# Kernel tuning notes

Measured on AMD Instinct MI355X. Metric: run time of the kernel, lower is better.

Reference implementation:

```python
import jax, jax.numpy as jnp
import numpy as np

NUM_HEADS = 8
CH_PER_HEAD = 32
NUM_GROUPS = 32
EPS = 1e-5
SCALE = CH_PER_HEAD ** (-0.25)


def setup_inputs() -> dict:
    key = jax.random.key(0)
    ks = jax.random.split(key, 6)
    B, C, H, W = 2, 256, 64, 64
    hid = NUM_HEADS * CH_PER_HEAD  # 256
    s = 1.0 / np.sqrt(C)
    return {
        "x": jax.random.normal(ks[0], (B, C, H, W), dtype=jnp.float32),
        "gamma": jnp.ones((C,), jnp.float32),
        "beta": jnp.zeros((C,), jnp.float32),
        "wq": jax.random.normal(ks[1], (hid, C), jnp.float32) * s,
        "bq": jnp.zeros((hid,), jnp.float32),
        "wk": jax.random.normal(ks[2], (hid, C), jnp.float32) * s,
        "bk": jnp.zeros((hid,), jnp.float32),
        "wv": jax.random.normal(ks[3], (hid, C), jnp.float32) * s,
        "bv": jnp.zeros((hid,), jnp.float32),
        "wout": jax.random.normal(ks[4], (C, hid), jnp.float32) * s,
        "bout": jnp.zeros((C,), jnp.float32),
    }


def _group_norm(x, gamma, beta):
    b, c, h, w = x.shape
    xg = x.reshape(b, NUM_GROUPS, c // NUM_GROUPS, h, w)
    mu = jnp.mean(xg, axis=(2, 3, 4), keepdims=True)
    var = jnp.var(xg, axis=(2, 3, 4), keepdims=True)
    xg = (xg - mu) * jax.lax.rsqrt(var + EPS)
    return xg.reshape(b, c, h, w) * gamma[None, :, None, None] + beta[None, :, None, None]


def reference(x, gamma, beta, wq, bq, wk, bk, wv, bv, wout, bout):
    b, c, h, w = x.shape
    n = h * w
    x_n = _group_norm(x, gamma, beta).reshape(b, c, n)  # b c n (self-attention: embedding = x_n)
    # 1x1 convs == pointwise linear over the channel dim
    q = jnp.einsum('oc,bcn->bon', wq, x_n) + bq[None, :, None]
    k = jnp.einsum('oc,bcn->bon', wk, x_n) + bk[None, :, None]
    v = jnp.einsum('oc,bcn->bon', wv, x_n) + bv[None, :, None]
    # split heads: b (h d) n -> b h d n
    d = CH_PER_HEAD
    q = q.reshape(b, NUM_HEADS, d, n)
    k = k.reshape(b, NUM_HEADS, d, n)
    v = v.reshape(b, NUM_HEADS, d, n)
    attn = jax.nn.softmax(jnp.einsum('bhdi,bhdj->bhij', q * SCALE, k * SCALE), axis=-1)
    out = jnp.einsum('bhij,bhdj->bhdi', attn, v).reshape(b, NUM_HEADS * d, n)
    out = jnp.einsum('oc,bcn->bon', wout, out) + bout[None, :, None]
    out = out.reshape(b, -1, h, w)
    return x + out  # shapes match -> residual
```

## Files before the change

### kernel.cpp

```cpp
#include <hip/hip_runtime.h>
#include <hip/hip_bf16.h>
#include <stdint.h>

typedef unsigned short u16;
typedef float f32x4 __attribute__((ext_vector_type(4)));
typedef float f32x16 __attribute__((ext_vector_type(16)));
typedef short bf16x8 __attribute__((ext_vector_type(8)));

#define NSP 4096
#define CDIM 256
#define HID 256
#define NH 8
#define DH 32
#define NG 32
#define CPG 8
#define BATCH 2
#define SPLIT 4
#define GN_EPS 1e-5f
#define QK2_SCALE 0.25503488f

#define MFMA32(A, B, C) __builtin_amdgcn_mfma_f32_32x32x16_bf16(A, B, C, 0, 0, 0)
#define MFMA16(A, B, C) __builtin_amdgcn_mfma_f32_16x16x32_bf16(A, B, C, 0, 0, 0)

__device__ __forceinline__ float bf2f(u16 u) {
    union { uint32_t i; float f; } v; v.i = ((uint32_t)u) << 16; return v.f;
}
__device__ __forceinline__ u16 f2bf(float f) {
    union { float f; uint32_t i; } v; v.f = f;
    uint32_t b = v.i;
    return (u16)((b + 0x7FFFu + ((b >> 16) & 1u)) >> 16);
}

__device__ __forceinline__ void gload16(const u16* g, u16* lds) {
    __builtin_amdgcn_global_load_lds(
        (const __attribute__((address_space(1))) uint32_t*)g,
        (__attribute__((address_space(3))) uint32_t*)lds, 16, 0, 0);
}

__device__ __forceinline__ void pl32swap(uint32_t& a, uint32_t& b) {
    asm("v_permlane32_swap_b32 %0, %1" : "+v"(a), "+v"(b));
}

__global__ void gn_stats(const float* __restrict__ x, float* __restrict__ stats,
                         const float* __restrict__ wq, const float* __restrict__ wk,
                         const float* __restrict__ wv, const float* __restrict__ wout,
                         u16* __restrict__ wcat) {
    int blk = blockIdx.x;
#pragma unroll
    for (int i = 0; i < 16; i++) {
        int idx = blk * 4096 + i * 256 + threadIdx.x;
        const float* src = (idx < 65536) ? wq : (idx < 131072) ? wk : (idx < 196608) ? wv : wout;
        wcat[idx] = f2bf(src[idx & 65535]);
    }
    const float4* base = (const float4*)(x + (size_t)blk * (CPG * NSP));
    float s = 0.f, ss = 0.f;
    for (int i = threadIdx.x; i < (CPG * NSP) / 4; i += 256) {
        float4 v = base[i];
        s  += v.x + v.y + v.z + v.w;
        ss += v.x * v.x + v.y * v.y + v.z * v.z + v.w * v.w;
    }
    for (int m = 1; m < 64; m <<= 1) { s += __shfl_xor(s, m, 64); ss += __shfl_xor(ss, m, 64); }
    __shared__ float ls[4], lss[4];
    int w = threadIdx.x >> 6;
    if ((threadIdx.x & 63) == 0) { ls[w] = s; lss[w] = ss; }
    __syncthreads();
    if (threadIdx.x == 0) {
        float S = ls[0] + ls[1] + ls[2] + ls[3];
        float SS = lss[0] + lss[1] + lss[2] + lss[3];
        float mean = S / (float)(CPG * NSP);
        float var = SS / (float)(CPG * NSP) - mean * mean;
        stats[2 * blk] = mean;
        stats[2 * blk + 1] = rsqrtf(var + GN_EPS);
    }
}

__global__ void gn_apply(const float* __restrict__ x, const float* __restrict__ stats,
                         const float* __restrict__ gamma, const float* __restrict__ beta,
                         u16* __restrict__ xn) {
    __shared__ u16 tile[64][72];
    int n0 = blockIdx.x * 64, c0 = blockIdx.y * 64, b = blockIdx.z;
    int t = threadIdx.x;
    int nl = t & 63, cq = t >> 6;
#pragma unroll
    for (int i = 0; i < 16; i++) {
        int cl = i * 4 + cq;
        int c = c0 + cl;
        int g = c >> 3;
        float mean = stats[2 * (b * NG + g)];
        float rstd = stats[2 * (b * NG + g) + 1];
        float v = x[((size_t)b * CDIM + c) * NSP + n0 + nl];
        v = (v - mean) * rstd * gamma[c] + beta[c];
        tile[cl][nl] = f2bf(v);
    }
    __syncthreads();
    int nr = t >> 2, cc = (t & 3) * 16;
    uint4 o0, o1;
    u16* p0 = (u16*)&o0; u16* p1 = (u16*)&o1;
#pragma unroll
    for (int j = 0; j < 8; j++) { p0[j] = tile[cc + j][nr]; p1[j] = tile[cc + 8 + j][nr]; }
    size_t orow = ((size_t)b * NSP + n0 + nr) * CDIM + c0 + cc;
    *(uint4*)(xn + orow) = o0;
    *(uint4*)(xn + orow + 8) = o1;
}

__global__ __launch_bounds__(256) void gemm_qkv(
    const u16* __restrict__ A, const u16* __restrict__ wcat,
    const float* __restrict__ bq, const float* __restrict__ bk, const float* __restrict__ bv,
    u16* __restrict__ qb, u16* __restrict__ kfb, u16* __restrict__ vfb) {
    __shared__ u16 As[128 * 64];
    __shared__ u16 Bs[128 * 64];
    int bz = blockIdx.z;
    const u16* Ab = A + (size_t)bz * NSP * CDIM;
    int n0 = blockIdx.x * 128, m0 = blockIdx.y * 128;
    int seg = n0 >> 8;
    int t = threadIdx.x, lane = t & 63, w = t >> 6;
    int wr = w >> 1, wc = w & 1;
    f32x4 acc[4][4] = {};

    int srow = w * 8 + (lane >> 3);
    int scol = (lane & 7) * 8;
    const u16* asrc = Ab + (size_t)(m0 + srow) * CDIM + scol;
    const u16* bsrc = wcat + (size_t)(n0 + srow) * CDIM + scol;
    u16* albase = As + w * 512;
    u16* blbase = Bs + w * 512;

    int frow = lane & 15, fcol = (lane >> 4) * 8;

    for (int k0 = 0; k0 < CDIM; k0 += 64) {
        __syncthreads();
#pragma unroll
        for (int ro = 0; ro < 4; ro++) {
            gload16(asrc + (size_t)ro * 32 * CDIM + k0, albase + ro * 2048);
            gload16(bsrc + (size_t)ro * 32 * CDIM + k0, blbase + ro * 2048);
        }
        asm volatile("s_waitcnt vmcnt(0)" ::: "memory");
        __syncthreads();
#pragma unroll
        for (int kk = 0; kk < 2; kk++) {
            bf16x8 af[4], bfv[4];
#pragma unroll
            for (int i = 0; i < 4; i++) {
                af[i]  = *(bf16x8*)&As[(wr * 64 + i * 16 + frow) * 64 + kk * 32 + fcol];
                bfv[i] = *(bf16x8*)&Bs[(wc * 64 + i * 16 + frow) * 64 + kk * 32 + fcol];
            }
#pragma unroll
            for (int i = 0; i < 4; i++)
#pragma unroll
                for (int j = 0; j < 4; j++)
                    acc[i][j] = MFMA16(af[i], bfv[j], acc[i][j]);
        }
    }

    const float* bias = (seg == 0) ? bq : (seg == 1) ? bk : bv;
    int r4 = (lane >> 4) * 4, cx = lane & 15;
#pragma unroll
    for (int i = 0; i < 4; i++) {
        int rbase = m0 + wr * 64 + i * 16 + r4;
#pragma unroll
        for (int j = 0; j < 4; j++) {
            int col = n0 + wc * 64 + j * 16 + cx;
            int cb = col & 255;
            float bb = bias[cb];
            if (seg == 0) {
#pragma unroll
                for (int r = 0; r < 4; r++)
                    qb[(size_t)bz * NSP * HID + (size_t)(rbase + r) * HID + cb] = f2bf(acc[i][j][r] + bb);
            } else if (seg == 1) {
                int h2 = cb >> 5;
                int f = 2 * ((rbase >> 5) & 1) + ((cb >> 4) & 1);
                size_t kt = ((size_t)(bz * NH + h2) * 64 + (rbase >> 6)) * 2048
                          + (size_t)f * 512 + ((rbase & 31) + (((cb >> 3) & 1) << 5)) * 8 + (cb & 7);
#pragma unroll
                for (int r = 0; r < 4; r++)
                    kfb[kt + r * 8] = f2bf((acc[i][j][r] + bb) * QK2_SCALE);
            } else {
                int h2 = cb >> 5, d = cb & 31;
                int jc = (rbase >> 3) & 7;
                size_t vt = ((size_t)(bz * NH + h2) * 64 + (rbase >> 6)) * 2048
                          + (size_t)(jc >> 1) * 512 + (d + ((jc & 1) << 5)) * 8 + (rbase & 7);
                uint2 pkd;
                pkd.x = ((uint32_t)f2bf(acc[i][j][1] + bb) << 16) | f2bf(acc[i][j][0] + bb);
                pkd.y = ((uint32_t)f2bf(acc[i][j][3] + bb) << 16) | f2bf(acc[i][j][2] + bb);
                *(uint2*)(vfb + vt) = pkd;
            }
        }
    }
}

__global__ __launch_bounds__(256) void gemm_out(
    const u16* __restrict__ A,
    const u16* __restrict__ B, long sB,
    const float* __restrict__ bias,
    const float* __restrict__ resid, long sR,
    float* __restrict__ outp, long sO,
    int N) {
    __shared__ u16 As[64][72];
    __shared__ u16 Bs[64][72];
    int bz = blockIdx.z;
    B += (size_t)bz * sB;
    int m0 = blockIdx.y * 64, n0 = blockIdx.x * 64;
    int t = threadIdx.x, lane = t & 63, w = t >> 6;
    int wm = (w >> 1) * 32, wn = (w & 1) * 32;
    f32x4 acc[2][2] = {};

    int sr = t >> 2;
    int sc1 = (t & 3) * 8, sc2 = sc1 + 32;

    uint4 av0 = *(const uint4*)(A + (size_t)(m0 + sr) * CDIM + sc1);
    uint4 av1 = *(const uint4*)(A + (size_t)(m0 + sr) * CDIM + sc2);
    uint4 bv0 = *(const uint4*)(B + (size_t)(n0 + sr) * CDIM + sc1);
    uint4 bv1 = *(const uint4*)(B + (size_t)(n0 + sr) * CDIM + sc2);

    for (int k0 = 0; k0 < CDIM; k0 += 64) {
        __syncthreads();
        *(uint4*)&As[sr][sc1] = av0;
        *(uint4*)&As[sr][sc2] = av1;
        *(uint4*)&Bs[sr][sc1] = bv0;
        *(uint4*)&Bs[sr][sc2] = bv1;
        __syncthreads();
        if (k0 + 64 < CDIM) {
            av0 = *(const uint4*)(A + (size_t)(m0 + sr) * CDIM + k0 + 64 + sc1);
            av1 = *(const uint4*)(A + (size_t)(m0 + sr) * CDIM + k0 + 64 + sc2);
            bv0 = *(const uint4*)(B + (size_t)(n0 + sr) * CDIM + k0 + 64 + sc1);
            bv1 = *(const uint4*)(B + (size_t)(n0 + sr) * CDIM + k0 + 64 + sc2);
        }
#pragma unroll
        for (int ks = 0; ks < 2; ks++) {
            bf16x8 af[2], bfr[2];
#pragma unroll
            for (int i = 0; i < 2; i++) {
                af[i]  = *(bf16x8*)&As[wm + i * 16 + (lane & 15)][ks * 32 + (lane >> 4) * 8];
                bfr[i] = *(bf16x8*)&Bs[wn + i * 16 + (lane & 15)][ks * 32 + (lane >> 4) * 8];
            }
#pragma unroll
            for (int i = 0; i < 2; i++)
#pragma unroll
                for (int j = 0; j < 2; j++)
                    acc[i][j] = MFMA16(af[i], bfr[j], acc[i][j]);
        }
    }

    int r4 = (lane >> 4) * 4, cx = lane & 15;
#pragma unroll
    for (int i = 0; i < 2; i++)
#pragma unroll
        for (int j = 0; j < 2; j++) {
            int rbase = m0 + wm + i * 16 + r4;
            int cbase = n0 + wn + j * 16 + cx;
#pragma unroll
            for (int r = 0; r < 4; r++) {
                int row = rbase + r, col = cbase;
                outp[(size_t)bz * sO + (size_t)row * N + col] =
                    acc[i][j][r] + bias[row] + resid[(size_t)bz * sR + (size_t)row * N + col];
            }
        }
}

__global__ __launch_bounds__(256, 4) void attn_kernel(
    const u16* __restrict__ q, const u16* __restrict__ kfb,
    const u16* __restrict__ vfb, u16* __restrict__ po, float* __restrict__ zz) {
    __shared__ float Ls[4][32];
    int h = blockIdx.y;
    int bz = blockIdx.z;
    int b = bz >> 2, sp = bz & 3;
    int kv0 = sp * (NSP / SPLIT);
    int t = threadIdx.x, lane = t & 63, w = t >> 6;
    int ql = lane & 31, hi = lane >> 5;
    int q0 = blockIdx.x * 128 + w * 32;

    const u16* qbp = q + (size_t)b * NSP * HID + (size_t)(q0 + ql) * HID + h * DH + hi * 8;
    bf16x8 qf0 = *(const bf16x8*)(qbp);
    bf16x8 qf1 = *(const bf16x8*)(qbp + 16);

    size_t tbase = ((size_t)(b * NH + h) * 64 + (kv0 >> 6)) * 2048 + (size_t)lane * 8;
    const u16* kp = kfb + tbase;
    const u16* vp = vfb + tbase;

#define LOADKF(kd, it) { \
    kd[0] = *(const bf16x8*)(kp + (size_t)(it) * 2048);        \
    kd[1] = *(const bf16x8*)(kp + (size_t)(it) * 2048 + 512);  \
    kd[2] = *(const bf16x8*)(kp + (size_t)(it) * 2048 + 1024); \
    kd[3] = *(const bf16x8*)(kp + (size_t)(it) * 2048 + 1536); }
#define LOADVF(vd, it) { \
    vd[0] = *(const bf16x8*)(vp + (size_t)(it) * 2048);        \
    vd[1] = *(const bf16x8*)(vp + (size_t)(it) * 2048 + 512);  \
    vd[2] = *(const bf16x8*)(vp + (size_t)(it) * 2048 + 1024); \
    vd[3] = *(const bf16x8*)(vp + (size_t)(it) * 2048 + 1536); }

    f32x16 kzero = {};
    f32x16 oacc = {};
    float l0 = 0.f, l1 = 0.f;

    auto process = [&](const bf16x8 (&kf)[4], const bf16x8 (&vf)[4]) {
#pragma unroll
        for (int tt = 0; tt < 2; tt++) {
            __builtin_amdgcn_s_setprio(1);
            f32x16 st = MFMA32(kf[2 * tt], qf0, kzero);
            st = MFMA32(kf[2 * tt + 1], qf1, st);
            __builtin_amdgcn_s_setprio(0);
            uint32_t pk[8];
#pragma unroll
            for (int j = 0; j < 8; j++) {
                float p0 = __builtin_amdgcn_exp2f(st[2 * j]);
                float p1 = __builtin_amdgcn_exp2f(st[2 * j + 1]);
                float ps = p0 + p1;
                if (j & 1) l1 += ps; else l0 += ps;
                uint32_t dd;
                asm("v_cvt_pk_bf16_f32 %0, %1, %2" : "=v"(dd) : "v"(p0), "v"(p1));
                pk[j] = dd;
            }
#pragma unroll
            for (int c = 0; c < 2; c++) {
                uint32_t a0 = pk[4 * c + 0], b0 = pk[4 * c + 2];
                uint32_t a1 = pk[4 * c + 1], b1 = pk[4 * c + 3];
                pl32swap(a0, b0);
                pl32swap(a1, b1);
                union { uint32_t u[4]; bf16x8 v8; } fr;
                fr.u[0] = a0; fr.u[1] = a1; fr.u[2] = b0; fr.u[3] = b1;
                __builtin_amdgcn_s_setprio(1);
                oacc = MFMA32(fr.v8, vf[2 * tt + c], oacc);
                __builtin_amdgcn_s_setprio(0);
            }
        }
    };

    const int NT = (NSP / SPLIT) / 64;
    bf16x8 ka[4], kc[4], va[4];
    LOADKF(ka, 0);
    for (int it = 0; it < NT; it += 2) {
        LOADVF(va, it);
        LOADKF(kc, it + 1);
        process(ka, va);
        LOADVF(va, it + 1);
        int n2 = (it + 2 < NT) ? it + 2 : 0;
        LOADKF(ka, n2);
        process(kc, va);
    }
#undef LOADKF
#undef LOADVF

    float l = l0 + l1;
    l += __shfl_xor(l, 32);
    Ls[w][ql] = 1.0f / l;
    if (hi == 0) zz[(((size_t)bz * NH + h) * NSP) + q0 + ql] = __log2f(l);
    u16* pob = po + ((((size_t)bz * NH + h) * NSP) + q0) * DH + ql;
#pragma unroll
    for (int r = 0; r < 16; r++) {
        int qq = (r & 3) + 8 * (r >> 2) + 4 * hi;
        pob[(size_t)qq * DH] = f2bf(oacc[r] * Ls[w][qq]);
    }
}

__global__ __launch_bounds__(256) void combine_kernel(
    const u16* __restrict__ po, const float* __restrict__ zz, u16* __restrict__ ao) {
    int idx = blockIdx.x * 256 + threadIdx.x;
    int c8 = idx & 31;
    int n  = (idx >> 5) & (NSP - 1);
    int b  = idx >> 17;
    int h  = c8 >> 2;
    int dp = (c8 & 3) * 8;

    float z[SPLIT];
    size_t base[SPLIT];
    float M = -3e38f;
#pragma unroll
    for (int s = 0; s < SPLIT; s++) {
        base[s] = ((((size_t)(b * SPLIT + s) * NH + h) * NSP) + n);
        z[s] = zz[base[s]];
        M = fmaxf(M, z[s]);
    }
    float wsum = 0.f, acc[8] = {};
#pragma unroll
    for (int s = 0; s < SPLIT; s++) {
        float ww = __builtin_amdgcn_exp2f(z[s] - M);
        wsum += ww;
        uint4 o = *(const uint4*)(po + base[s] * DH + dp);
        const u16* op = (const u16*)&o;
#pragma unroll
        for (int j = 0; j < 8; j++) acc[j] += bf2f(op[j]) * ww;
    }
    float inv = 1.0f / wsum;
    uint4 r;
    u16* rp = (u16*)&r;
#pragma unroll
    for (int j = 0; j < 8; j++) rp[j] = f2bf(acc[j] * inv);
    *(uint4*)(ao + (((size_t)b * NSP + n) * HID) + h * DH + dp) = r;
}

extern "C" void kernel_launch(void* const* d_in, const int* in_sizes, int n_in,
                              void* d_out, int out_size, void* d_ws, size_t ws_size,
                              hipStream_t stream) {
    const float* x     = (const float*)d_in[0];
    const float* gamma = (const float*)d_in[1];
    const float* beta  = (const float*)d_in[2];
    const float* wq    = (const float*)d_in[3];
    const float* bq    = (const float*)d_in[4];
    const float* wk    = (const float*)d_in[5];
    const float* bk    = (const float*)d_in[6];
    const float* wv    = (const float*)d_in[7];
    const float* bv    = (const float*)d_in[8];
    const float* wout  = (const float*)d_in[9];
    const float* bout  = (const float*)d_in[10];
    float* out = (float*)d_out;

    char* ws = (char*)d_ws;
    float* stats = (float*)ws;
    u16* wq_b = (u16*)(ws + 4096);
    u16* wo_b = wq_b + 3 * 65536;
    u16* xn = wo_b + 65536;
    u16* qb = xn + (size_t)BATCH * NSP * CDIM;
    u16* kfb = qb + (size_t)BATCH * NSP * HID;
    u16* vfb = kfb + (size_t)BATCH * NH * 64 * 2048;
    u16* aob = vfb + (size_t)BATCH * NH * 64 * 2048;
    u16* pob = aob + (size_t)BATCH * NSP * HID;
    float* zzb = (float*)(pob + (size_t)SPLIT * BATCH * NH * NSP * DH);

    const long sQ = (long)NSP * HID;
    const long sOut = (long)CDIM * NSP;

    gn_stats<<<BATCH * NG, 256, 0, stream>>>(x, stats, wq, wk, wv, wout, wq_b);
    gn_apply<<<dim3(NSP / 64, CDIM / 64, BATCH), 256, 0, stream>>>(x, stats, gamma, beta, xn);

    gemm_qkv<<<dim3(768 / 128, NSP / 128, BATCH), 256, 0, stream>>>(
        xn, wq_b, bq, bk, bv, qb, kfb, vfb);

    attn_kernel<<<dim3(NSP / 128, NH, BATCH * SPLIT), 256, 0, stream>>>(qb, kfb, vfb, pob, zzb);
    combine_kernel<<<(BATCH * NSP * HID / 8) / 256, 256, 0, stream>>>(pob, zzb, aob);

    gemm_out<<<dim3(NSP / 64, CDIM / 64, BATCH), 256, 0, stream>>>(
        wo_b, aob, sQ, bout, x, sOut, out, sOut, NSP);
}
```

Before: 93.42 us.

## Process two query tiles per wave in attention to reuse K/V fragments

Each wave now handles 64 queries (two 32-row tiles) instead of 32, so every K and V fragment loaded from global memory feeds twice as many MFMAs. The grid along the query axis is halved and the launch-bounds occupancy hint drops from 4 to 3 blocks to make room for the extra accumulators and Q fragments. This cuts K/V load traffic per unit of work and adds independent MFMA chains for latency hiding, at the cost of higher register pressure, lower occupancy and fewer blocks in flight.

```diff
diff --git a/kernel.cpp b/kernel.cpp
--- a/kernel.cpp
+++ b/kernel.cpp
@@ -256,21 +256,23 @@
         }
 }
 
-__global__ __launch_bounds__(256, 4) void attn_kernel(
+__global__ __launch_bounds__(256, 3) void attn_kernel(
     const u16* __restrict__ q, const u16* __restrict__ kfb,
     const u16* __restrict__ vfb, u16* __restrict__ po, float* __restrict__ zz) {
-    __shared__ float Ls[4][32];
+    __shared__ float Ls[4][64];
     int h = blockIdx.y;
     int bz = blockIdx.z;
     int b = bz >> 2, sp = bz & 3;
     int kv0 = sp * (NSP / SPLIT);
     int t = threadIdx.x, lane = t & 63, w = t >> 6;
     int ql = lane & 31, hi = lane >> 5;
-    int q0 = blockIdx.x * 128 + w * 32;
+    int q0 = blockIdx.x * 256 + w * 64;
 
     const u16* qbp = q + (size_t)b * NSP * HID + (size_t)(q0 + ql) * HID + h * DH + hi * 8;
-    bf16x8 qf0 = *(const bf16x8*)(qbp);
-    bf16x8 qf1 = *(const bf16x8*)(qbp + 16);
+    bf16x8 qa0 = *(const bf16x8*)(qbp);
+    bf16x8 qa1 = *(const bf16x8*)(qbp + 16);
+    bf16x8 qb0 = *(const bf16x8*)(qbp + 32 * HID);
+    bf16x8 qb1 = *(const bf16x8*)(qbp + 32 * HID + 16);
 
     size_t tbase = ((size_t)(b * NH + h) * 64 + (kv0 >> 6)) * 2048 + (size_t)lane * 8;
     const u16* kp = kfb + tbase;
@@ -288,39 +290,47 @@
     vd[3] = *(const bf16x8*)(vp + (size_t)(it) * 2048 + 1536); }
 
     f32x16 kzero = {};
-    f32x16 oacc = {};
-    float l0 = 0.f, l1 = 0.f;
+    f32x16 oacc_a = {}, oacc_b = {};
+    float la0 = 0.f, la1 = 0.f, lb0 = 0.f, lb1 = 0.f;
+
+    auto softpv = [&](f32x16& st, const bf16x8 (&vf)[4], int tt, f32x16& oacc,
+                      float& l0, float& l1) {
+        uint32_t pk[8];
+#pragma unroll
+        for (int j = 0; j < 8; j++) {
+            float p0 = __builtin_amdgcn_exp2f(st[2 * j]);
+            float p1 = __builtin_amdgcn_exp2f(st[2 * j + 1]);
+            float ps = p0 + p1;
+            if (j & 1) l1 += ps; else l0 += ps;
+            uint32_t dd;
+            asm("v_cvt_pk_bf16_f32 %0, %1, %2" : "=v"(dd) : "v"(p0), "v"(p1));
+            pk[j] = dd;
+        }
+#pragma unroll
+        for (int c = 0; c < 2; c++) {
+            uint32_t a0 = pk[4 * c + 0], b0 = pk[4 * c + 2];
+            uint32_t a1 = pk[4 * c + 1], b1 = pk[4 * c + 3];
+            pl32swap(a0, b0);
+            pl32swap(a1, b1);
+            union { uint32_t u[4]; bf16x8 v8; } fr;
+            fr.u[0] = a0; fr.u[1] = a1; fr.u[2] = b0; fr.u[3] = b1;
+            __builtin_amdgcn_s_setprio(1);
+            oacc = MFMA32(fr.v8, vf[2 * tt + c], oacc);
+            __builtin_amdgcn_s_setprio(0);
+        }
+    };
 
     auto process = [&](const bf16x8 (&kf)[4], const bf16x8 (&vf)[4]) {
 #pragma unroll
         for (int tt = 0; tt < 2; tt++) {
             __builtin_amdgcn_s_setprio(1);
-            f32x16 st = MFMA32(kf[2 * tt], qf0, kzero);
-            st = MFMA32(kf[2 * tt + 1], qf1, st);
+            f32x16 st_a = MFMA32(kf[2 * tt], qa0, kzero);
+            st_a = MFMA32(kf[2 * tt + 1], qa1, st_a);
+            f32x16 st_b = MFMA32(kf[2 * tt], qb0, kzero);
+            st_b = MFMA32(kf[2 * tt + 1], qb1, st_b);
             __builtin_amdgcn_s_setprio(0);
-            uint32_t pk[8];
-#pragma unroll
-            for (int j = 0; j < 8; j++) {
-                float p0 = __builtin_amdgcn_exp2f(st[2 * j]);
-                float p1 = __builtin_amdgcn_exp2f(st[2 * j + 1]);
-                float ps = p0 + p1;
-                if (j & 1) l1 += ps; else l0 += ps;
-                uint32_t dd;
-                asm("v_cvt_pk_bf16_f32 %0, %1, %2" : "=v"(dd) : "v"(p0), "v"(p1));
-                pk[j] = dd;
-            }
-#pragma unroll
-            for (int c = 0; c < 2; c++) {
-                uint32_t a0 = pk[4 * c + 0], b0 = pk[4 * c + 2];
-                uint32_t a1 = pk[4 * c + 1], b1 = pk[4 * c + 3];
-                pl32swap(a0, b0);
-                pl32swap(a1, b1);
-                union { uint32_t u[4]; bf16x8 v8; } fr;
-                fr.u[0] = a0; fr.u[1] = a1; fr.u[2] = b0; fr.u[3] = b1;
-                __builtin_amdgcn_s_setprio(1);
-                oacc = MFMA32(fr.v8, vf[2 * tt + c], oacc);
-                __builtin_amdgcn_s_setprio(0);
-            }
+            softpv(st_a, vf, tt, oacc_a, la0, la1);
+            softpv(st_b, vf, tt, oacc_b, lb0, lb1);
         }
     };
 
@@ -339,15 +349,22 @@
 #undef LOADKF
 #undef LOADVF
 
-    float l = l0 + l1;
-    l += __shfl_xor(l, 32);
-    Ls[w][ql] = 1.0f / l;
-    if (hi == 0) zz[(((size_t)bz * NH + h) * NSP) + q0 + ql] = __log2f(l);
+    float la = la0 + la1;
+    float lb = lb0 + lb1;
+    la += __shfl_xor(la, 32);
+    lb += __shfl_xor(lb, 32);
+    Ls[w][ql] = 1.0f / la;
+    Ls[w][32 + ql] = 1.0f / lb;
+    if (hi == 0) {
+        zz[(((size_t)bz * NH + h) * NSP) + q0 + ql] = __log2f(la);
+        zz[(((size_t)bz * NH + h) * NSP) + q0 + 32 + ql] = __log2f(lb);
+    }
     u16* pob = po + ((((size_t)bz * NH + h) * NSP) + q0) * DH + ql;
 #pragma unroll
     for (int r = 0; r < 16; r++) {
         int qq = (r & 3) + 8 * (r >> 2) + 4 * hi;
-        pob[(size_t)qq * DH] = f2bf(oacc[r] * Ls[w][qq]);
+        pob[(size_t)qq * DH] = f2bf(oacc_a[r] * Ls[w][qq]);
+        pob[(size_t)(32 + qq) * DH] = f2bf(oacc_b[r] * Ls[w][32 + qq]);
     }
 }
 
@@ -424,7 +441,7 @@
     gemm_qkv<<<dim3(768 / 128, NSP / 128, BATCH), 256, 0, stream>>>(
         xn, wq_b, bq, bk, bv, qb, kfb, vfb);
 
-    attn_kernel<<<dim3(NSP / 128, NH, BATCH * SPLIT), 256, 0, stream>>>(qb, kfb, vfb, pob, zzb);
+    attn_kernel<<<dim3(NSP / 256, NH, BATCH * SPLIT), 256, 0, stream>>>(qb, kfb, vfb, pob, zzb);
     combine_kernel<<<(BATCH * NSP * HID / 8) / 256, 256, 0, stream>>>(pob, zzb, aob);
 
     gemm_out<<<dim3(NSP / 64, CDIM / 64, BATCH), 256, 0, stream>>>(
```

Result: faster. 91.45 us (-2.1%).
